# Optimization experiments

Measured on AMD Instinct MI355X. Metric: run time of the kernel, lower is better.

The kernel has to match this reference:

```python
import jax, jax.numpy as jnp
import numpy as np

H, DN, DR, DV = 16, 128, 64, 128   # heads, nope dim, rope dim, v dim
QR, KR = 1536, 512                 # q / kv lora ranks
HI, DI, TOPK = 32, 128, 512        # indexer heads, indexer head dim, index_topk

def rmsnorm(x, w, eps=1e-6):
    return x * jax.lax.rsqrt(jnp.mean(x * x, -1, keepdims=True) + eps) * w

def layernorm(x, w, b, eps=1e-5):
    m = jnp.mean(x, -1, keepdims=True)
    v = jnp.mean((x - m) ** 2, -1, keepdims=True)
    return (x - m) * jax.lax.rsqrt(v + eps) * w + b

def rope_interleaved(x, cos, sin):
    # x: [b,s,h,d]; cos,sin: [s,d//2]; pairs are (x[2j], x[2j+1])
    x0, x1 = x[..., 0::2], x[..., 1::2]
    c, s = cos[None, :, None, :], sin[None, :, None, :]
    return jnp.stack([x0 * c - x1 * s, x0 * s + x1 * c], -1).reshape(x.shape)

def rope_half(x, cos, sin):
    # non-interleaved variant: pairs are (x[j], x[j+d/2]); output = [real_half, imag_half]
    d = x.shape[-1] // 2
    x0, x1 = x[..., :d], x[..., d:]
    c, s = cos[None, :, None, :], sin[None, :, None, :]
    return jnp.concatenate([x0 * c - x1 * s, x0 * s + x1 * c], -1)

def setup_inputs():
    key = jax.random.key(0)
    B, S, DM = 1, 2048, 2048
    ks = jax.random.split(key, 10)
    w = lambda k, shape: jax.random.normal(k, shape, jnp.float32) * 0.02
    inp = {
        'hidden_states': jax.random.normal(ks[0], (B, S, DM), jnp.float32),
        'wq_a': w(ks[1], (QR, DM)),
        'q_norm_w': jnp.ones((QR,), jnp.float32),
        'wq_b': w(ks[2], (H * (DN + DR), QR)),
        'wkv_a': w(ks[3], (KR + DR, DM)),
        'kv_norm_w': jnp.ones((KR,), jnp.float32),
        'wkv_b': w(ks[4], (H * (DN + DV), KR)),
        'wo': w(ks[5], (DM, H * DV)),
        'idx_wq_b': w(ks[6], (HI * DI, QR)),
        'idx_wk': w(ks[7], (DI, DM)),
        'idx_kn_w': jnp.ones((DI,), jnp.float32),
        'idx_kn_b': jnp.zeros((DI,), jnp.float32),
        'idx_wproj': w(ks[8], (HI, DM)),
    }
    ang = jnp.arange(S, dtype=jnp.float32)[:, None] / (10000.0 ** (jnp.arange(0, DR, 2, dtype=jnp.float32) / DR))[None, :]
    inp['freqs_cos'], inp['freqs_sin'] = jnp.cos(ang), jnp.sin(ang)
    inp['mask'] = jnp.broadcast_to(
        jnp.where(jnp.tril(jnp.ones((S, S), bool)), 0.0, -jnp.inf).astype(jnp.float32), (B, S, S))
    return inp

def reference(hidden_states, freqs_cos, freqs_sin, mask, wq_a, q_norm_w, wq_b, wkv_a,
              kv_norm_w, wkv_b, wo, idx_wq_b, idx_wk, idx_kn_w, idx_kn_b, idx_wproj):
    B, S, DM = hidden_states.shape
    # --- MLA low-rank Q/KV projections ---
    qr = rmsnorm(hidden_states @ wq_a.T, q_norm_w)                       # [B,S,QR]
    q = (qr @ wq_b.T).reshape(B, S, H, DN + DR)
    q_pe = rope_interleaved(q[..., DN:], freqs_cos, freqs_sin)
    q = jnp.concatenate([q[..., :DN], q_pe], -1)                         # [B,S,H,192]
    kv_all = hidden_states @ wkv_a.T                                     # [B,S,KR+DR]
    kv = rmsnorm(kv_all[..., :KR], kv_norm_w)
    k_pe = rope_interleaved(kv_all[..., KR:][:, :, None, :], freqs_cos, freqs_sin)  # [B,S,1,DR]
    kvp = (kv @ wkv_b.T).reshape(B, S, H, DN + DV)
    k = jnp.concatenate([kvp[..., :DN], jnp.broadcast_to(k_pe, (B, S, H, DR))], -1)
    v = kvp[..., DN:]                                                    # [B,S,H,DV]
    scores = jnp.einsum('bshd,bthd->bsht', q, k) * (DN + DR) ** -0.5
    # --- indexer: relu-weighted scores -> top-k token set ---
    qi = (qr @ idx_wq_b.T).reshape(B, S, HI, DI)
    qi = jnp.concatenate([rope_half(qi[..., :DR], freqs_cos, freqs_sin), qi[..., DR:]], -1)
    ki = layernorm(hidden_states @ idx_wk.T, idx_kn_w, idx_kn_b)         # [B,S,DI]
    ki_pe = rope_half(ki[..., :DR][:, :, None, :], freqs_cos, freqs_sin)[:, :, 0, :]
    ki = jnp.concatenate([ki_pe, ki[..., DR:]], -1)
    wts = (hidden_states @ idx_wproj.T) * HI ** -0.5                     # [B,S,HI]
    iscores = jax.nn.relu(jnp.einsum('bshd,btd->bsht', qi, ki) * DI ** -0.5) * wts[..., None]
    index_scores = iscores.sum(2) + mask                                 # [B,S,S]
    topk_idx = jax.lax.top_k(index_scores, TOPK)[1]                      # [B,S,TOPK]
    index_mask = jnp.full((B, S, S), -jnp.inf, jnp.float32)
    index_mask = index_mask.at[jnp.arange(B)[:, None, None],
                               jnp.arange(S)[None, :, None], topk_idx].set(0.0)
    # --- sparse-masked attention ---
    scores = scores + (index_mask + mask)[:, :, None, :]
    probs = jax.nn.softmax(scores, axis=-1)
    out = jnp.einsum('bsht,bthd->bshd', probs, v).reshape(B, S, H * DV)
    return out @ wo.T
```

## Files before the change

### kernel.cpp

```cpp
#include <hip/hip_runtime.h>
#include <stdint.h>

typedef unsigned int uint;
typedef unsigned short u16;
typedef unsigned long long u64;

typedef float  f32x4 __attribute__((ext_vector_type(4)));
typedef uint   u32x4 __attribute__((ext_vector_type(4)));
typedef u16    u16x4 __attribute__((ext_vector_type(4)));
typedef u16    u16x8 __attribute__((ext_vector_type(8)));
typedef __bf16 bf16x8 __attribute__((ext_vector_type(8)));

#define DEV static __device__ __forceinline__
#define MFMA(a,b,c) __builtin_amdgcn_mfma_f32_16x16x32_bf16((a),(b),(c),0,0,0)
#define GLDS(src,dst) __builtin_amdgcn_global_load_lds((const __attribute__((address_space(1))) void*)(src),(__attribute__((address_space(3))) void*)(dst),16,0,0)

DEV u16 f2bf(float x){ union{float f;uint u;} v; v.f=x; return (u16)((v.u + 0x7fffu + ((v.u>>16)&1u))>>16); }
DEV float bf2f(u16 b){ union{uint u;float f;} v; v.u=((uint)b)<<16; return v.f; }
DEV int imin(int a,int b){ return a<b?a:b; }

__global__ void cvt_all(
    const float* __restrict__ hs, const float* __restrict__ wqa, const float* __restrict__ iwqb,
    const float* __restrict__ iwk, const float* __restrict__ iwp,
    const float* __restrict__ wqbw, const float* __restrict__ wkva, const float* __restrict__ wkvb,
    const float* __restrict__ wow,
    u16* __restrict__ hid_hi, u16* __restrict__ hid_lo, u16* __restrict__ wqa_hi, u16* __restrict__ wqa_lo,
    u16* __restrict__ iwqb_hi, u16* __restrict__ iwqb_lo, u16* __restrict__ kiwp_hi, u16* __restrict__ kiwp_lo,
    u16* __restrict__ wqb_b, u16* __restrict__ wkva_b, u16* __restrict__ wkvb_b, u16* __restrict__ wo_b)
{
  int i = blockIdx.x*blockDim.x + threadIdx.x;
  int st = gridDim.x*blockDim.x;
  for(; i < 6537216; i += st){
    const float* src; u16 *dh, *dl=nullptr; int j; bool split;
    if(i < 1048576){ src=hs;   dh=hid_hi;  dl=hid_lo;  j=i;         split=true; }
    else if(i < 1835008){ src=wqa;  dh=wqa_hi;  dl=wqa_lo;  j=i-1048576; split=true; }
    else if(i < 3407872){ src=iwqb; dh=iwqb_hi; dl=iwqb_lo; j=i-1835008; split=true; }
    else if(i < 3473408){ src=iwk;  dh=kiwp_hi; dl=kiwp_lo; j=i-3407872; split=true; }
    else if(i < 3489792){ src=iwp;  dh=kiwp_hi+128*2048; dl=kiwp_lo+128*2048; j=i-3473408; split=true; }
    else if(i < 4669440){ src=wqbw; dh=wqb_b;  j=i-3489792; split=false; }
    else if(i < 4964352){ src=wkva; dh=wkva_b; j=i-4669440; split=false; }
    else if(i < 5488640){ src=wkvb; dh=wkvb_b; j=i-4964352; split=false; }
    else               { src=wow;  dh=wo_b;   j=i-5488640; split=false; }
    f32x4 x = reinterpret_cast<const f32x4*>(src)[j];
    u16x4 h;
    #pragma unroll
    for(int k=0;k<4;k++) h[k]=f2bf(x[k]);
    reinterpret_cast<u16x4*>(dh)[j]=h;
    if(split){
      u16x4 l;
      #pragma unroll
      for(int k=0;k<4;k++) l[k]=f2bf(x[k]-bf2f(h[k]));
      reinterpret_cast<u16x4*>(dl)[j]=l;
    }
  }
}

template<int BK>
DEV void stageT(const u16* __restrict__ gbase, int ld, int row0, int maxrow, int k0, u16* lds){
  int tid = threadIdx.x, w = tid>>6, l = tid&63;
  if(BK==32){
    #pragma unroll
    for(int j=0;j<2;j++){
      int seg = w + j*4;
      int row = seg*16 + (l>>2);
      int gr = row0 + row; if(gr > maxrow) gr = maxrow;
      GLDS(gbase + (size_t)gr*ld + k0 + (l&3)*8, lds + seg*512);
    }
  } else {
    #pragma unroll
    for(int j=0;j<4;j++){
      int c = w + j*4;
      int row = c*8 + (l>>3);
      int gr = row0 + row; if(gr > maxrow) gr = maxrow;
      GLDS(gbase + (size_t)gr*ld + k0 + (l&7)*8, lds + c*512);
    }
  }
}

template<int SPLIT, int BK>
__global__ __launch_bounds__(256,2) void gemm_glds(
    const u16* __restrict__ Ah, const u16* __restrict__ Al, int lda,
    const u16* __restrict__ Bh, const u16* __restrict__ Bl, int ldb,
    float* __restrict__ C, int ldc, int M, int N, int K)
{
  __shared__ u16 sAh[128*BK];
  __shared__ u16 sBh[128*BK];
  __shared__ u16 sAl[SPLIT?128*BK:8];
  __shared__ u16 sBl[SPLIT?128*BK:8];
  const int tid = threadIdx.x;
  const int w = tid>>6, l = tid&63;
  const int wr = w>>1, wc = w&1;
  const int l15 = l&15, l16 = l>>4;

  int gx = gridDim.x;
  int nwg = gx*gridDim.y;
  int orig = blockIdx.x + gx*blockIdx.y;
  int qq = nwg>>3, rr = nwg&7, xc = orig&7, oo = orig>>3;
  int wg = (xc<rr ? xc*(qq+1) : rr*(qq+1)+(xc-rr)*qq) + oo;
  int m0 = (wg/gx)*128, n0 = (wg%gx)*128;

  int kz = K/(int)gridDim.z;
  int kbeg = blockIdx.z*kz;

  f32x4 acc[4][4];
  #pragma unroll
  for(int m=0;m<4;m++)
    #pragma unroll
    for(int n=0;n<4;n++) acc[m][n] = f32x4{0.f,0.f,0.f,0.f};

  for(int k0=kbeg; k0<kbeg+kz; k0+=BK){
    __syncthreads();
    stageT<BK>(Ah, lda, m0, M-1, k0, sAh);
    stageT<BK>(Bh, ldb, n0, N-1, k0, sBh);
    if(SPLIT){
      stageT<BK>(Al, lda, m0, M-1, k0, sAl);
      stageT<BK>(Bl, ldb, n0, N-1, k0, sBl);
    }
    asm volatile("s_waitcnt vmcnt(0)" ::: "memory");
    __syncthreads();
    #pragma unroll
    for(int kk=0;kk<BK/32;kk++){
      bf16x8 ah[4], bh[4];
      #pragma unroll
      for(int m=0;m<4;m++) ah[m] = *reinterpret_cast<const bf16x8*>(&sAh[(wr*64+m*16+l15)*BK + kk*32 + l16*8]);
      #pragma unroll
      for(int n=0;n<4;n++) bh[n] = *reinterpret_cast<const bf16x8*>(&sBh[(wc*64+n*16+l15)*BK + kk*32 + l16*8]);
      #pragma unroll
      for(int m=0;m<4;m++)
        #pragma unroll
        for(int n=0;n<4;n++) acc[m][n] = MFMA(ah[m], bh[n], acc[m][n]);
      if(SPLIT){
        bf16x8 t[4];
        #pragma unroll
        for(int n=0;n<4;n++) t[n] = *reinterpret_cast<const bf16x8*>(&sBl[(wc*64+n*16+l15)*BK + kk*32 + l16*8]);
        #pragma unroll
        for(int m=0;m<4;m++)
          #pragma unroll
          for(int n=0;n<4;n++) acc[m][n] = MFMA(ah[m], t[n], acc[m][n]);
        #pragma unroll
        for(int m=0;m<4;m++) t[m] = *reinterpret_cast<const bf16x8*>(&sAl[(wr*64+m*16+l15)*BK + kk*32 + l16*8]);
        #pragma unroll
        for(int m=0;m<4;m++)
          #pragma unroll
          for(int n=0;n<4;n++) acc[m][n] = MFMA(t[m], bh[n], acc[m][n]);
      }
    }
  }
  float* Cp = C + (size_t)blockIdx.z*M*ldc;
  #pragma unroll
  for(int m=0;m<4;m++){
    int row = m0 + wr*64 + m*16 + l16*4;
    #pragma unroll
    for(int n=0;n<4;n++){
      int col = n0 + wc*64 + n*16 + l15;
      if(col < N){
        #pragma unroll
        for(int r=0;r<4;r++){
          int rrow = row + r;
          if(rrow < M) Cp[(size_t)rrow*ldc + col] = acc[m][n][r];
        }
      }
    }
  }
}

__global__ __launch_bounds__(256) void rmsnorm_qr_split(
    const float* __restrict__ in, const float* __restrict__ w,
    u16* __restrict__ hi, u16* __restrict__ lo)
{
  int s = blockIdx.x, tid = threadIdx.x;
  __shared__ float red[4];
  const float* x = in + (size_t)s*1536;
  const size_t plane = 2048ull*1536;
  float xv[6]; float ss=0.f;
  #pragma unroll
  for(int i=0;i<6;i++){ int c = tid+i*256; xv[i] = x[c] + x[plane+c]; ss += xv[i]*xv[i]; }
  #pragma unroll
  for(int o=32;o>0;o>>=1) ss += __shfl_down(ss,o,64);
  if((tid&63)==0) red[tid>>6]=ss;
  __syncthreads();
  float total = red[0]+red[1]+red[2]+red[3];
  float scale = rsqrtf(total*(1.0f/1536.0f) + 1e-6f);
  #pragma unroll
  for(int i=0;i<6;i++){
    int c = tid + i*256;
    float vv = xv[i]*scale*w[c];
    u16 hv = f2bf(vv);
    hi[(size_t)s*1536+c]=hv;
    lo[(size_t)s*1536+c]=f2bf(vv - bf2f(hv));
  }
}

__global__ __launch_bounds__(256) void kv_norm_rope(
    const float* __restrict__ kva, const float* __restrict__ w,
    const float* __restrict__ fcos, const float* __restrict__ fsin,
    u16* __restrict__ kvb, float* __restrict__ kpe)
{
  int s = blockIdx.x, tid = threadIdx.x;
  __shared__ float red[4];
  const size_t plane = 2048ull*576;
  float xv[2]={0.f,0.f};
  #pragma unroll
  for(int c=0;c<4;c++){
    const float* xp = kva + (size_t)c*plane + (size_t)s*576;
    xv[0]+=xp[tid]; xv[1]+=xp[tid+256];
  }
  float ss = xv[0]*xv[0]+xv[1]*xv[1];
  #pragma unroll
  for(int o=32;o>0;o>>=1) ss += __shfl_down(ss,o,64);
  if((tid&63)==0) red[tid>>6]=ss;
  __syncthreads();
  float total = red[0]+red[1]+red[2]+red[3];
  float scale = rsqrtf(total*(1.0f/512.0f)+1e-6f);
  #pragma unroll
  for(int i=0;i<2;i++){ int c=tid+i*256; kvb[(size_t)s*512+c]=f2bf(xv[i]*scale*w[c]); }
  if(tid<32){
    float x0=0.f, x1=0.f;
    #pragma unroll
    for(int c=0;c<4;c++){
      const float* xp = kva + (size_t)c*plane + (size_t)s*576;
      x0 += xp[512+2*tid]; x1 += xp[513+2*tid];
    }
    float c0=fcos[(size_t)s*32+tid], s_=fsin[(size_t)s*32+tid];
    kpe[(size_t)s*64+2*tid]   = x0*c0 - x1*s_;
    kpe[(size_t)s*64+2*tid+1] = x0*s_ + x1*c0;
  }
}

__global__ __launch_bounds__(256) void rope_q_cvt(const float* __restrict__ qpre,
    const float* __restrict__ fcos, const float* __restrict__ fsin, u16* __restrict__ qb)
{
  int s = blockIdx.x;
  const float* rowp = qpre + (size_t)s*3072;
  u16* op = qb + (size_t)s*3072;
  for(int idx=threadIdx.x; idx<3072; idx+=256){
    int hh = idx/192, d = idx - hh*192;
    float vv;
    if(d < 128) vv = rowp[hh*192 + d];
    else{
      int i2 = (d-128)>>1;
      float c0 = fcos[(size_t)s*32+i2], s_ = fsin[(size_t)s*32+i2];
      float x0 = rowp[hh*192 + 128 + 2*i2], x1 = rowp[hh*192 + 129 + 2*i2];
      vv = ((d&1)==0) ? (x0*c0 - x1*s_) : (x0*s_ + x1*c0);
    }
    op[idx] = f2bf(vv);
  }
}

__global__ __launch_bounds__(256) void qi_rope_split(const float* __restrict__ qpre,
    const float* __restrict__ fcos, const float* __restrict__ fsin,
    u16* __restrict__ hi, u16* __restrict__ lo)
{
  int s = blockIdx.x;
  const float* rowp = qpre + (size_t)s*4096;
  for(int idx=threadIdx.x; idx<4096; idx+=256){
    int hh = idx>>7, d = idx&127;
    const float* hb = rowp + (hh<<7);
    float vv;
    if(d<32){ float c0=fcos[(size_t)s*32+d], s_=fsin[(size_t)s*32+d]; vv = hb[d]*c0 - hb[d+32]*s_; }
    else if(d<64){ int i2=d-32; float c0=fcos[(size_t)s*32+i2], s_=fsin[(size_t)s*32+i2]; vv = hb[i2]*s_ + hb[d]*c0; }
    else vv = hb[d];
    u16 hv = f2bf(vv);
    hi[(size_t)s*4096+idx]=hv;
    lo[(size_t)s*4096+idx]=f2bf(vv - bf2f(hv));
  }
}

__global__ __launch_bounds__(128) void ki_ln_rope_split(
    const float* __restrict__ kpre, const float* __restrict__ w, const float* __restrict__ bb,
    const float* __restrict__ fcos, const float* __restrict__ fsin,
    u16* __restrict__ hi, u16* __restrict__ lo, float* __restrict__ wts_out)
{
  int s = blockIdx.x, tid = threadIdx.x;
  __shared__ float red[2];
  __shared__ float ybuf[128];
  const size_t plane = 2048ull*160;
  float x = 0.f;
  #pragma unroll
  for(int c=0;c<8;c++) x += kpre[(size_t)c*plane + (size_t)s*160 + tid];
  if(tid<32){
    float ws = 0.f;
    #pragma unroll
    for(int c=0;c<8;c++) ws += kpre[(size_t)c*plane + (size_t)s*160 + 128 + tid];
    wts_out[(size_t)s*160 + 128 + tid] = ws;
  }
  float v = x;
  #pragma unroll
  for(int o=32;o>0;o>>=1) v += __shfl_down(v,o,64);
  if((tid&63)==0) red[tid>>6]=v;
  __syncthreads();
  float mean = (red[0]+red[1])*(1.f/128.f);
  __syncthreads();
  float dx = x - mean;
  v = dx*dx;
  #pragma unroll
  for(int o=32;o>0;o>>=1) v += __shfl_down(v,o,64);
  if((tid&63)==0) red[tid>>6]=v;
  __syncthreads();
  float var = (red[0]+red[1])*(1.f/128.f);
  float y = dx*rsqrtf(var+1e-5f)*w[tid] + bb[tid];
  ybuf[tid]=y;
  __syncthreads();
  float r;
  if(tid<32){ float c0=fcos[(size_t)s*32+tid], s_=fsin[(size_t)s*32+tid]; r = ybuf[tid]*c0 - ybuf[tid+32]*s_; }
  else if(tid<64){ int i2=tid-32; float c0=fcos[(size_t)s*32+i2], s_=fsin[(size_t)s*32+i2]; r = ybuf[i2]*s_ + ybuf[tid]*c0; }
  else r = y;
  u16 hv=f2bf(r);
  hi[(size_t)s*128+tid]=hv;
  lo[(size_t)s*128+tid]=f2bf(r-bf2f(hv));
}

__global__ __launch_bounds__(256) void transpose_assemble(const float* __restrict__ kvp,
    const float* __restrict__ kpe, u16* __restrict__ vt, u16* __restrict__ kb){
  __shared__ u16 T[64*136];
  int s0 = blockIdx.x*64, h = blockIdx.y;
  int tid = threadIdx.x;
  for(int idx=tid; idx<64*192; idx+=256){
    int r = idx/192, d = idx - r*192;
    float val = (d<128) ? kvp[(size_t)(s0+r)*4096 + h*256 + d] : kpe[(size_t)(s0+r)*64 + (d-128)];
    kb[((size_t)(s0+r)*16 + h)*192 + d] = f2bf(val);
  }
  #pragma unroll
  for(int i=0;i<8;i++){
    int ch = i*256 + tid;
    int r = ch>>5, cc = ch&31;
    f32x4 x = *reinterpret_cast<const f32x4*>(&kvp[(size_t)(s0+r)*4096 + h*256 + 128 + cc*4]);
    u16x4 y;
    #pragma unroll
    for(int j=0;j<4;j++) y[j] = f2bf(x[j]);
    *reinterpret_cast<u16x4*>(&T[r*136 + cc*4]) = y;
  }
  __syncthreads();
  #pragma unroll
  for(int i=0;i<4;i++){
    int ch = i*256 + tid;
    int d = ch>>3, sc = ch&7;
    u16x8 y;
    #pragma unroll
    for(int j=0;j<8;j++) y[j] = T[(sc*8+j)*136 + d];
    *reinterpret_cast<u16x8*>(&vt[((size_t)h*128 + d)*2048 + s0 + sc*8]) = y;
  }
}

DEV void isc_pass64(const u16* __restrict__ Q, const u16* __restrict__ Kb,
                    f32x4 (&sc)[2][2], int wm, int wn, int l15, int l16){
  #pragma unroll
  for(int ks=0;ks<4;ks++){
    bf16x8 a[2], b[2];
    #pragma unroll
    for(int m=0;m<2;m++){
      int row = wm*32 + m*16 + l15;
      a[m] = *reinterpret_cast<const bf16x8*>(&Q[row*128 + ((((ks<<2)+l16) ^ (row&7))<<3)]);
    }
    #pragma unroll
    for(int n=0;n<2;n++){
      int row = wn*32 + n*16 + l15;
      b[n] = *reinterpret_cast<const bf16x8*>(&Kb[row*128 + ((((ks<<2)+l16) ^ (row&7))<<3)]);
    }
    #pragma unroll
    for(int m=0;m<2;m++)
      #pragma unroll
      for(int n=0;n<2;n++) sc[m][n] = MFMA(a[m], b[n], sc[m][n]);
  }
}

__global__ __launch_bounds__(512,4) void idx_scores7(
    const u16* __restrict__ qih, const u16* __restrict__ qil,
    const u16* __restrict__ kih, const u16* __restrict__ kil,
    const float* __restrict__ wts,
    float* __restrict__ p0, float* __restrict__ p1, float* __restrict__ p2, float* __restrict__ p3)
{
  __shared__ u16 Kh[128*128];
  __shared__ u16 Kl[128*128];
  __shared__ u16 Qb[64*128];
  int orig = blockIdx.x;
  int bid = (orig&7)*136 + (orig>>3);
  int tileIdx = bid>>2, hg = bid&3;
  int si=0, t=tileIdx;
  #pragma unroll 1
  for(; si<32; si++){ int cnt=(si+2)>>1; if(t<cnt) break; t-=cnt; }
  int s0 = si*64, t0 = t*128;
  float* plane = (hg==0)?p0:(hg==1)?p1:(hg==2)?p2:p3;
  float* outp = plane + (size_t)tileIdx*8192;
  int h0 = hg*8;
  int tid=threadIdx.x, w=tid>>6, l=tid&63;
  int wm=w>>2, wn=w&3, l15=l&15, l16=l>>4;
  const float cscale = 0.015625f;
  #pragma unroll
  for(int rnd=0;rnd<4;rnd++){
    int cid = rnd*512 + w*64 + l;
    int row = cid>>4, cc = cid&15;
    int scc = cc ^ (row&7);
    GLDS(kih + (size_t)(t0+row)*128 + scc*8, Kh + rnd*4096 + w*512);
    GLDS(kil + (size_t)(t0+row)*128 + scc*8, Kl + rnd*4096 + w*512);
  }
  #pragma unroll
  for(int rnd=0;rnd<2;rnd++){
    int cid = rnd*512 + w*64 + l;
    int row = cid>>4, cc = cid&15;
    int scc = cc ^ (row&7);
    GLDS(qih + (size_t)(s0+row)*4096 + h0*128 + scc*8, Qb + rnd*4096 + w*512);
  }
  asm volatile("s_waitcnt vmcnt(0)" ::: "memory");
  __syncthreads();
  f32x4 accI[2][2], sc[2][2];
  #pragma unroll
  for(int m=0;m<2;m++) for(int n=0;n<2;n++) accI[m][n] = f32x4{0.f,0.f,0.f,0.f};
  for(int s=0;s<16;s++){
    const u16* Q = Qb;
    if((s&1)==0){
      #pragma unroll
      for(int m=0;m<2;m++) for(int n=0;n<2;n++) sc[m][n] = f32x4{0.f,0.f,0.f,0.f};
      isc_pass64(Q, Kh, sc, wm, wn, l15, l16);
      isc_pass64(Q, Kl, sc, wm, wn, l15, l16);
    } else {
      isc_pass64(Q, Kh, sc, wm, wn, l15, l16);
      int hh = h0 + (s>>1);
      #pragma unroll
      for(int m=0;m<2;m++)
        #pragma unroll
        for(int r=0;r<4;r++){
          float wv = wts[(size_t)(s0+wm*32+m*16+l16*4+r)*160 + 128 + hh]*cscale;
          #pragma unroll
          for(int n=0;n<2;n++) accI[m][n][r] += fmaxf(sc[m][n][r],0.f)*wv;
        }
    }
    __syncthreads();
    int nxt = s+1;
    if(nxt < 16){
      const u16* src = (nxt&1) ? qil : qih;
      int hh = h0 + (nxt>>1);
      #pragma unroll
      for(int rnd=0;rnd<2;rnd++){
        int cid = rnd*512 + w*64 + l;
        int row = cid>>4, cc = cid&15;
        int scc = cc ^ (row&7);
        GLDS(src + (size_t)(s0+row)*4096 + hh*128 + scc*8, Qb + rnd*4096 + w*512);
      }
      asm volatile("s_waitcnt vmcnt(0)" ::: "memory");
      __syncthreads();
    }
  }
  #pragma unroll
  for(int m=0;m<2;m++)
    #pragma unroll
    for(int n=0;n<2;n++)
      #pragma unroll
      for(int r=0;r<4;r++)
        outp[(wm*32+m*16+l16*4+r)*128 + wn*32 + n*16 + l15] = accI[m][n][r];
}

DEV uint fkey(float f){ union{float f;uint u;} v; v.f=f; return (v.u & 0x80000000u) ? ~v.u : (v.u | 0x80000000u); }

__global__ __launch_bounds__(256) void topk_mask(
    const float* __restrict__ p0, const float* __restrict__ p1,
    const float* __restrict__ p2, const float* __restrict__ p3, u64* __restrict__ bits)
{
  int s = blockIdx.x;
  int n = s+1;
  int tid = threadIdx.x;
  if(n <= 512){
    for(int wI=tid; wI<32; wI+=256){
      u64 m=0; int base=wI*64;
      if(base < n){ int cnt=n-base; m = (cnt>=64)? ~0ull : ((1ull<<cnt)-1ull); }
      bits[(size_t)s*32+wI]=m;
    }
    return;
  }
  __shared__ float row[2048];
  __shared__ uint hist[256];
  __shared__ uint sh_B, sh_k;
  __shared__ uint wcnt[32];
  int si = s>>6, sr = s&63;
  size_t triBase = (size_t)(((si+1)*(si+1))>>2);
  for(int c=tid; c<n; c+=256){
    size_t off = (triBase + (size_t)(c>>7))*8192 + (size_t)sr*128 + (c&127);
    row[c] = p0[off]+p1[off]+p2[off]+p3[off];
  }
  __syncthreads();
  uint prefix=0, k=512;
  for(int shift=24; shift>=0; shift-=8){
    hist[tid]=0;
    __syncthreads();
    for(int t2=tid;t2<n;t2+=256){
      uint u = fkey(row[t2]);
      bool ok = (shift==24) || ((u>>(shift+8)) == (prefix>>(shift+8)));
      if(ok) atomicAdd(&hist[(u>>shift)&255u],1u);
    }
    __syncthreads();
    for(int offd=1; offd<256; offd<<=1){
      uint add = (tid+offd<256)? hist[tid+offd] : 0u;
      __syncthreads();
      hist[tid] += add;
      __syncthreads();
    }
    uint nxtv = (tid<255)? hist[tid+1] : 0u;
    if(hist[tid]>=k && nxtv<k){ sh_B=(uint)tid; sh_k = k - nxtv; }
    __syncthreads();
    prefix |= sh_B<<shift;
    k = sh_k;
    __syncthreads();
  }
  uint thr = prefix;
  if(tid<32) wcnt[tid]=0;
  __syncthreads();
  int nw = (n+63)>>6;
  if(tid < nw){
    int base=tid*64, end = base+64; if(end>n) end=n;
    uint c=0;
    for(int t2=base;t2<end;t2++) if(fkey(row[t2])==thr) c++;
    wcnt[tid]=c;
  }
  __syncthreads();
  if(tid==0){
    uint runv=0;
    for(int i=0;i<32;i++){ uint c=wcnt[i]; wcnt[i]=runv; runv+=c; }
  }
  __syncthreads();
  if(tid<32){
    u64 m=0; int base=tid*64;
    if(base<n){
      uint rank = wcnt[tid];
      int end = base+64; if(end>n) end=n;
      for(int t2=base;t2<end;t2++){
        uint u = fkey(row[t2]);
        if(u>thr) m |= (1ull<<(t2-base));
        else if(u==thr){ if(rank<k) m |= (1ull<<(t2-base)); rank++; }
      }
    }
    bits[(size_t)s*32+tid]=m;
  }
}

__global__ __launch_bounds__(256,3) void flash_attn(
    const u16* __restrict__ q, const u16* __restrict__ k, const u16* __restrict__ vt,
    const u64* __restrict__ bits, u16* __restrict__ o,
    u16* __restrict__ Opart, float* __restrict__ ml)
{
  __shared__ u16 Ks[64*192];
  __shared__ u16 Vt[128*64];
  __shared__ u16 Pl[64*72];
  int h = blockIdx.y;
  int pp = blockIdx.x;
  int sblk=0, chunk=0;
  for(int i=0;i<32;i++){
    int sb = 31-i; int ncc = (sb>>3)+1;
    if(pp < ncc){ sblk=sb; chunk=pp; break; }
    pp -= ncc;
  }
  int nc = (sblk>>3)+1, ntiles = sblk+1, s0 = sblk*64;
  int tid=threadIdx.x, w=tid>>6, l=tid&63;
  int l15=l&15, l16=l>>4;
  const float sscale = 0.07216878364870323f;
  bf16x8 qf[6];
  #pragma unroll
  for(int ks=0;ks<6;ks++)
    qf[ks] = *reinterpret_cast<const bf16x8*>(&q[((size_t)(s0+w*16+l15)*16 + h)*192 + ks*32 + l16*8]);
  f32x4 Oa[8];
  #pragma unroll
  for(int n=0;n<8;n++) Oa[n] = f32x4{0.f,0.f,0.f,0.f};
  float mrun[4], lrun[4];
  #pragma unroll
  for(int r=0;r<4;r++){ mrun[r]=-__builtin_inff(); lrun[r]=0.f; }
  int tt0 = chunk*8, tt1 = imin(tt0+8, ntiles);
  for(int tt=tt0; tt<tt1; tt++){
    int t0 = tt*64;
    __syncthreads();
    #pragma unroll
    for(int rnd=0;rnd<6;rnd++){
      int cid = rnd*256 + w*64 + l;
      int row = cid/24, cc = cid - row*24;
      int scc = cc ^ (row&7);
      GLDS(k + ((size_t)(t0+row)*16 + h)*192 + scc*8, Ks + rnd*2048 + w*512);
    }
    #pragma unroll
    for(int rnd=0;rnd<4;rnd++){
      int cid = rnd*256 + w*64 + l;
      int row = cid>>3, cc = cid&7;
      int scc = cc ^ (row&7);
      GLDS(vt + ((size_t)h*128 + row)*2048 + t0 + scc*8, Vt + rnd*2048 + w*512);
    }
    asm volatile("s_waitcnt vmcnt(0)" ::: "memory");
    __syncthreads();
    f32x4 S[4];
    #pragma unroll
    for(int n=0;n<4;n++) S[n] = f32x4{0.f,0.f,0.f,0.f};
    #pragma unroll
    for(int ks=0;ks<6;ks++){
      bf16x8 b[4];
      #pragma unroll
      for(int n=0;n<4;n++){
        int row = n*16+l15;
        b[n] = *reinterpret_cast<const bf16x8*>(&Ks[row*192 + ((((ks<<2)+l16) ^ (row&7))<<3)]);
      }
      #pragma unroll
      for(int n=0;n<4;n++) S[n] = MFMA(qf[ks], b[n], S[n]);
    }
    #pragma unroll
    for(int r=0;r<4;r++){
      int srow = s0 + w*16 + l16*4 + r;
      u64 wrd = bits[(size_t)srow*32 + (t0>>6)];
      float mx = -__builtin_inff();
      #pragma unroll
      for(int n=0;n<4;n++){
        int bitp = n*16 + l15;
        int tcol = t0 + bitp;
        bool ok = (tcol <= srow) && ((wrd>>bitp)&1ull);
        float val = ok ? S[n][r]*sscale : -__builtin_inff();
        S[n][r] = val;
        mx = fmaxf(mx, val);
      }
      #pragma unroll
      for(int off=1;off<16;off<<=1) mx = fmaxf(mx, __shfl_xor(mx, off, 64));
      float mold = mrun[r];
      float mnew = fmaxf(mold, mx);
      bool inf0 = (mnew == -__builtin_inff());
      float alpha = inf0 ? 1.f : __expf(mold - mnew);
      float rs = 0.f;
      #pragma unroll
      for(int n=0;n<4;n++){
        float p = inf0 ? 0.f : __expf(S[n][r] - mnew);
        S[n][r] = p;
        rs += p;
      }
      #pragma unroll
      for(int off=1;off<16;off<<=1) rs += __shfl_xor(rs, off, 64);
      mrun[r]=mnew;
      lrun[r] = lrun[r]*alpha + rs;
      #pragma unroll
      for(int n=0;n<8;n++) Oa[n][r] *= alpha;
    }
    #pragma unroll
    for(int n=0;n<4;n++)
      #pragma unroll
      for(int r=0;r<4;r++)
        Pl[(w*16+l16*4+r)*72 + n*16+l15] = f2bf(S[n][r]);
    #pragma unroll
    for(int ks=0;ks<2;ks++){
      bf16x8 a = *reinterpret_cast<const bf16x8*>(&Pl[(w*16+l15)*72 + ks*32 + l16*8]);
      bf16x8 bb[8];
      #pragma unroll
      for(int n=0;n<8;n++){
        int d = n*16+l15;
        bb[n] = *reinterpret_cast<const bf16x8*>(&Vt[d*64 + ((((ks<<2)+l16) ^ (d&7))<<3)]);
      }
      #pragma unroll
      for(int n=0;n<8;n++) Oa[n] = MFMA(a, bb[n], Oa[n]);
    }
  }
  if(nc == 1){
    #pragma unroll
    for(int r=0;r<4;r++){
      int srow = s0 + w*16 + l16*4 + r;
      float inv = 1.f/lrun[r];
      #pragma unroll
      for(int n=0;n<8;n++)
        o[(size_t)srow*2048 + h*128 + n*16 + l15] = f2bf(Oa[n][r]*inv);
    }
  } else {
    int part = ((h*32 + sblk)<<2) + chunk;
    u16* Op = Opart + (size_t)part*8192;
    #pragma unroll
    for(int r=0;r<4;r++){
      int rit = w*16 + l16*4 + r;
      #pragma unroll
      for(int n=0;n<8;n++)
        Op[rit*128 + n*16 + l15] = f2bf(Oa[n][r]);
      if(l15==0){
        ml[(size_t)part*128 + rit*2]   = mrun[r];
        ml[(size_t)part*128 + rit*2+1] = lrun[r];
      }
    }
  }
}

__global__ __launch_bounds__(256) void flash_combine(
    const u16* __restrict__ Opart, const float* __restrict__ ml, u16* __restrict__ o)
{
  int b = blockIdx.x;
  int h = b/24, sblk = 8 + (b%24);
  int nc = (sblk>>3)+1;
  int tid = threadIdx.x;
  int r = tid>>2, dq = (tid&3)*32;
  int s0 = sblk*64;
  int pbase = (h*32+sblk)<<2;
  float m[4], lv[4], wgt[4];
  float M = -__builtin_inff();
  for(int c=0;c<nc;c++){
    m[c]  = ml[(size_t)(pbase+c)*128 + r*2];
    lv[c] = ml[(size_t)(pbase+c)*128 + r*2 + 1];
    if(lv[c] > 0.f) M = fmaxf(M, m[c]);
  }
  float L = 0.f;
  for(int c=0;c<nc;c++){
    wgt[c] = (lv[c] > 0.f) ? __expf(m[c]-M) : 0.f;
    L += lv[c]*wgt[c];
  }
  float inv = 1.f/L;
  for(int dd=0; dd<32; dd+=8){
    float accv[8];
    #pragma unroll
    for(int j=0;j<8;j++) accv[j]=0.f;
    for(int c=0;c<nc;c++){
      u16x8 pv = *reinterpret_cast<const u16x8*>(&Opart[(size_t)(pbase+c)*8192 + r*128 + dq + dd]);
      #pragma unroll
      for(int j=0;j<8;j++) accv[j] += wgt[c]*bf2f(pv[j]);
    }
    u16x8 ov;
    #pragma unroll
    for(int j=0;j<8;j++) ov[j] = f2bf(accv[j]*inv);
    *reinterpret_cast<u16x8*>(&o[(size_t)(s0+r)*2048 + h*128 + dq + dd]) = ov;
  }
}

extern "C" void kernel_launch(void* const* d_in, const int* in_sizes, int n_in,
                              void* d_out, int out_size, void* d_ws, size_t ws_size,
                              hipStream_t stream)
{
  (void)in_sizes; (void)n_in; (void)out_size;
  const float* hs   = (const float*)d_in[0];
  const float* wqa  = (const float*)d_in[1];
  const float* qnw  = (const float*)d_in[2];
  const float* wqbw = (const float*)d_in[3];
  const float* wkva = (const float*)d_in[4];
  const float* kvnw = (const float*)d_in[5];
  const float* wkvb = (const float*)d_in[6];
  const float* wow  = (const float*)d_in[7];
  const float* iwqb = (const float*)d_in[8];
  const float* iwk  = (const float*)d_in[9];
  const float* iknw = (const float*)d_in[10];
  const float* iknb = (const float*)d_in[11];
  const float* iwp  = (const float*)d_in[12];
  const float* fcos = (const float*)d_in[13];
  const float* fsin = (const float*)d_in[14];
  float* outp = (float*)d_out;

  char* base = (char*)d_ws;
  size_t off = 0;
  auto alloc = [&](size_t bytes)->char*{ char* p = base+off; off += (bytes+255)&~(size_t)255; return p; };
  u16* hid_hi = (u16*)alloc(2048ull*2048*2);
  u16* hid_lo = (u16*)alloc(2048ull*2048*2);
  u16* wqa_hi = (u16*)alloc(1536ull*2048*2);
  u16* wqa_lo = (u16*)alloc(1536ull*2048*2);
  u16* wqb_b  = (u16*)alloc(3072ull*1536*2);
  u16* wkva_b = (u16*)alloc(576ull*2048*2);
  u16* wkvb_b = (u16*)alloc(4096ull*512*2);
  u16* wo_b   = (u16*)alloc(2048ull*2048*2);
  u16* iwqb_hi= (u16*)alloc(4096ull*1536*2);
  u16* iwqb_lo= (u16*)alloc(4096ull*1536*2);
  u16* kiwp_hi= (u16*)alloc(160ull*2048*2);
  u16* kiwp_lo= (u16*)alloc(160ull*2048*2);
  float* kiwp_C=(float*)alloc(2048ull*160*4);
  u16* qr_hi  = (u16*)alloc(2048ull*1536*2);
  u16* qr_lo  = (u16*)alloc(2048ull*1536*2);
  u16* kv_b   = (u16*)alloc(2048ull*512*2);
  float* kpe  = (float*)alloc(2048ull*64*4);
  u16* k_b    = (u16*)alloc(2048ull*16*192*2);
  u16* v_t    = (u16*)alloc(16ull*128*2048*2);
  u16* ki_hi  = (u16*)alloc(2048ull*128*2);
  u16* ki_lo  = (u16*)alloc(2048ull*128*2);
  u64* bits   = (u64*)alloc(2048ull*32*8);
  u16* attn_b = (u16*)alloc(2048ull*2048*2);
  float* reg1 = (float*)alloc(2048ull*4096*4);
  if(ws_size < off) return;

  u16* q_b      = wqa_hi;
  u16* qi_hi    = hid_hi;
  u16* qi_lo    = iwqb_hi;
  float* ml     = (float*)qr_lo;
  float* qr_pre = reg1;
  float* q_pre  = reg1;
  float* kva_part = reg1;
  float* kvp    = reg1;
  float* kiwp_part = reg1;
  float* qi_pre = reg1;
  const size_t PLANE = 272ull*8192;
  float* ip0 = reg1;
  float* ip1 = reg1 + PLANE;
  float* ip2 = reg1 + 2*PLANE;
  float* ip3 = (float*)wqb_b;
  u16* Opart = (u16*)reg1;

  auto G1 = [&](const u16* A,int lda,const u16* B,int ldb,float* C,int ldc,int M,int N,int K,int z){
    dim3 g((unsigned)((N+127)/128), (unsigned)((M+127)/128), (unsigned)z);
    gemm_glds<0,64><<<g,256,0,stream>>>(A,nullptr,lda,B,nullptr,ldb,C,ldc,M,N,K);
  };
  auto G3 = [&](const u16* Ah,const u16* Al,int lda,const u16* Bh,const u16* Bl,int ldb,float* C,int ldc,int M,int N,int K,int z){
    dim3 g((unsigned)((N+127)/128), (unsigned)((M+127)/128), (unsigned)z);
    gemm_glds<1,32><<<g,256,0,stream>>>(Ah,Al,lda,Bh,Bl,ldb,C,ldc,M,N,K);
  };

  cvt_all<<<2048,256,0,stream>>>(hs,wqa,iwqb,iwk,iwp,wqbw,wkva,wkvb,wow,
      hid_hi,hid_lo,wqa_hi,wqa_lo,iwqb_hi,iwqb_lo,kiwp_hi,kiwp_lo,
      wqb_b,wkva_b,wkvb_b,wo_b);

  G3(hid_hi,hid_lo,2048, wqa_hi,wqa_lo,2048, qr_pre,1536, 2048,1536,2048, 2);
  rmsnorm_qr_split<<<2048,256,0,stream>>>(qr_pre, qnw, qr_hi, qr_lo);

  G1(qr_hi,1536, wqb_b,1536, q_pre,3072, 2048,3072,1536, 1);
  rope_q_cvt<<<2048,256,0,stream>>>(q_pre, fcos, fsin, q_b);

  G1(hid_hi,2048, wkva_b,2048, kva_part,576, 2048,576,2048, 4);
  kv_norm_rope<<<2048,256,0,stream>>>(kva_part, kvnw, fcos, fsin, kv_b, kpe);
  G1(kv_b,512, wkvb_b,512, kvp,4096, 2048,4096,512, 1);
  transpose_assemble<<<dim3(32,16),256,0,stream>>>(kvp, kpe, v_t, k_b);

  G3(hid_hi,hid_lo,2048, kiwp_hi,kiwp_lo,2048, kiwp_part,160, 2048,160,2048, 8);
  ki_ln_rope_split<<<2048,128,0,stream>>>(kiwp_part, iknw, iknb, fcos, fsin, ki_hi, ki_lo, kiwp_C);

  G3(qr_hi,qr_lo,1536, iwqb_hi,iwqb_lo,1536, qi_pre,4096, 2048,4096,1536, 1);
  qi_rope_split<<<2048,256,0,stream>>>(qi_pre, fcos, fsin, qi_hi, qi_lo);

  idx_scores7<<<1088,512,0,stream>>>(qi_hi, qi_lo, ki_hi, ki_lo, kiwp_C, ip0, ip1, ip2, ip3);
  topk_mask<<<2048,256,0,stream>>>(ip0, ip1, ip2, ip3, bits);

  flash_attn<<<dim3(80,16),256,0,stream>>>(q_b, k_b, v_t, bits, attn_b, Opart, ml);
  flash_combine<<<384,256,0,stream>>>(Opart, ml, attn_b);
  G1(attn_b,2048, wo_b,2048, outp,2048, 2048,2048,2048, 1);
}
```

Before: 532.7 us.

## Swizzle GEMM LDS layout, widen split-GEMM BK, skip unneeded softmax rescale

The GEMM global-to-LDS staging now XOR-swizzles 16-byte chunks within each row, and the fragment reads apply the matching swizzle, to cut LDS bank conflicts on the MFMA operand loads. The split (hi/lo) GEMM moves from BK=32 to BK=64, which doubles its LDS footprint but halves the number of K iterations and barriers. In the sparse attention online softmax, the alpha exponential and the rescale of the O accumulator now run only when the row max actually increases. That last change adds a per-row branch, but the shuffle reductions keep its condition uniform across each 16-lane group.

After: 491.8 us. 1.08x faster.

```diff
diff --git a/kernel.cpp b/kernel.cpp
--- a/kernel.cpp
+++ b/kernel.cpp
@@ -64,7 +64,8 @@
       int seg = w + j*4;
       int row = seg*16 + (l>>2);
       int gr = row0 + row; if(gr > maxrow) gr = maxrow;
-      GLDS(gbase + (size_t)gr*ld + k0 + (l&3)*8, lds + seg*512);
+      int u = (l&3) ^ ((l>>2)&3);
+      GLDS(gbase + (size_t)gr*ld + k0 + u*8, lds + seg*512);
     }
   } else {
     #pragma unroll
@@ -72,7 +73,8 @@
       int c = w + j*4;
       int row = c*8 + (l>>3);
       int gr = row0 + row; if(gr > maxrow) gr = maxrow;
-      GLDS(gbase + (size_t)gr*ld + k0 + (l&7)*8, lds + c*512);
+      int u = (l&7) ^ ((l>>3)&7);
+      GLDS(gbase + (size_t)gr*ld + k0 + u*8, lds + c*512);
     }
   }
 }
@@ -91,6 +93,7 @@
   const int w = tid>>6, l = tid&63;
   const int wr = w>>1, wc = w&1;
   const int l15 = l&15, l16 = l>>4;
+  const int UM = BK/8 - 1;
 
   int gx = gridDim.x;
   int nwg = gx*gridDim.y;
@@ -122,9 +125,15 @@
     for(int kk=0;kk<BK/32;kk++){
       bf16x8 ah[4], bh[4];
       #pragma unroll
-      for(int m=0;m<4;m++) ah[m] = *reinterpret_cast<const bf16x8*>(&sAh[(wr*64+m*16+l15)*BK + kk*32 + l16*8]);
-      #pragma unroll
-      for(int n=0;n<4;n++) bh[n] = *reinterpret_cast<const bf16x8*>(&sBh[(wc*64+n*16+l15)*BK + kk*32 + l16*8]);
+      for(int m=0;m<4;m++){
+        int row = wr*64+m*16+l15;
+        ah[m] = *reinterpret_cast<const bf16x8*>(&sAh[row*BK + ((kk*4+l16)^(row&UM))*8]);
+      }
+      #pragma unroll
+      for(int n=0;n<4;n++){
+        int row = wc*64+n*16+l15;
+        bh[n] = *reinterpret_cast<const bf16x8*>(&sBh[row*BK + ((kk*4+l16)^(row&UM))*8]);
+      }
       #pragma unroll
       for(int m=0;m<4;m++)
         #pragma unroll
@@ -132,13 +141,19 @@
       if(SPLIT){
         bf16x8 t[4];
         #pragma unroll
-        for(int n=0;n<4;n++) t[n] = *reinterpret_cast<const bf16x8*>(&sBl[(wc*64+n*16+l15)*BK + kk*32 + l16*8]);
+        for(int n=0;n<4;n++){
+          int row = wc*64+n*16+l15;
+          t[n] = *reinterpret_cast<const bf16x8*>(&sBl[row*BK + ((kk*4+l16)^(row&UM))*8]);
+        }
         #pragma unroll
         for(int m=0;m<4;m++)
           #pragma unroll
           for(int n=0;n<4;n++) acc[m][n] = MFMA(ah[m], t[n], acc[m][n]);
         #pragma unroll
-        for(int m=0;m<4;m++) t[m] = *reinterpret_cast<const bf16x8*>(&sAl[(wr*64+m*16+l15)*BK + kk*32 + l16*8]);
+        for(int m=0;m<4;m++){
+          int row = wr*64+m*16+l15;
+          t[m] = *reinterpret_cast<const bf16x8*>(&sAl[row*BK + ((kk*4+l16)^(row&UM))*8]);
+        }
         #pragma unroll
         for(int m=0;m<4;m++)
           #pragma unroll
@@ -613,9 +628,9 @@
       #pragma unroll
       for(int off=1;off<16;off<<=1) mx = fmaxf(mx, __shfl_xor(mx, off, 64));
       float mold = mrun[r];
-      float mnew = fmaxf(mold, mx);
+      bool new_max = mx > mold;
+      float mnew = new_max ? mx : mold;
       bool inf0 = (mnew == -__builtin_inff());
-      float alpha = inf0 ? 1.f : __expf(mold - mnew);
       float rs = 0.f;
       #pragma unroll
       for(int n=0;n<4;n++){
@@ -625,10 +640,15 @@
       }
       #pragma unroll
       for(int off=1;off<16;off<<=1) rs += __shfl_xor(rs, off, 64);
-      mrun[r]=mnew;
-      lrun[r] = lrun[r]*alpha + rs;
-      #pragma unroll
-      for(int n=0;n<8;n++) Oa[n][r] *= alpha;
+      if(new_max){
+        float alpha = __expf(mold - mnew);
+        mrun[r] = mnew;
+        lrun[r] = lrun[r]*alpha + rs;
+        #pragma unroll
+        for(int n=0;n<8;n++) Oa[n][r] *= alpha;
+      } else {
+        lrun[r] += rs;
+      }
     }
     #pragma unroll
     for(int n=0;n<4;n++)
@@ -787,7 +807,7 @@
   };
   auto G3 = [&](const u16* Ah,const u16* Al,int lda,const u16* Bh,const u16* Bl,int ldb,float* C,int ldc,int M,int N,int K,int z){
     dim3 g((unsigned)((N+127)/128), (unsigned)((M+127)/128), (unsigned)z);
-    gemm_glds<1,32><<<g,256,0,stream>>>(Ah,Al,lda,Bh,Bl,ldb,C,ldc,M,N,K);
+    gemm_glds<1,64><<<g,256,0,stream>>>(Ah,Al,lda,Bh,Bl,ldb,C,ldc,M,N,K);
   };
 
   cvt_all<<<2048,256,0,stream>>>(hs,wqa,iwqb,iwk,iwp,wqbw,wkva,wkvb,wow,
```
